# Performance work log

Hardware: AMD Instinct MI355X
Metric: run time of the kernel (lower is better)

## Reference

```python
import jax, jax.numpy as jnp
import numpy as np

N = 100000      # nodes
E = 1600000     # edges (avg degree 16)
IN = 128        # in_channels
OUT = 32        # out_channels -> hidden = 2*OUT = 64


def gcn_conv(x, src, dst, W, b):
    """PyG GCNConv: linear transform, add self loops, symmetric D^-1/2 (A+I) D^-1/2 aggregation."""
    n = x.shape[0]
    h = x @ W                                   # [N, out]
    # degree with self loops (all edge weights = 1)
    deg = jax.ops.segment_sum(jnp.ones(src.shape[0], h.dtype), dst, num_segments=n) + 1.0
    dinv = jax.lax.rsqrt(deg)                   # [N]
    norm = dinv[src] * dinv[dst]                # [E]
    agg = jax.ops.segment_sum(h[src] * norm[:, None], dst, num_segments=n)
    agg = agg + h * (dinv * dinv)[:, None]      # self-loop contribution
    return agg + b


def setup_inputs() -> dict:
    key = jax.random.key(0)
    ks = jax.random.split(key, 8)
    x = jax.random.normal(ks[0], (N, IN), jnp.float32)
    edge_index = jax.random.randint(ks[1], (2, E), 0, N, jnp.int32)
    H = 2 * OUT
    W1 = jax.random.normal(ks[2], (IN, H), jnp.float32) / jnp.sqrt(jnp.float32(IN))
    b1 = jnp.zeros((H,), jnp.float32)
    W_mu = jax.random.normal(ks[3], (H, OUT), jnp.float32) / jnp.sqrt(jnp.float32(H))
    b_mu = jnp.zeros((OUT,), jnp.float32)
    W_logstd = jax.random.normal(ks[4], (H, OUT), jnp.float32) / jnp.sqrt(jnp.float32(H))
    b_logstd = jnp.zeros((OUT,), jnp.float32)
    return {"x": x, "edge_index": edge_index, "W1": W1, "b1": b1,
            "W_mu": W_mu, "b_mu": b_mu, "W_logstd": W_logstd, "b_logstd": b_logstd}


def reference(x, edge_index, W1, b1, W_mu, b_mu, W_logstd, b_logstd):
    src, dst = edge_index[0], edge_index[1]
    h = jax.nn.relu(gcn_conv(x, src, dst, W1, b1))          # [N, 2*OUT]
    mu = gcn_conv(h, src, dst, W_mu, b_mu)                  # [N, OUT]
    logstd = gcn_conv(h, src, dst, W_logstd, b_logstd)      # [N, OUT]
    return mu, logstd
```

## Files before the change

kernel.cpp:

```cpp
#include <hip/hip_runtime.h>
#include <hip/hip_fp16.h>

#define IN_C 128
#define H 64
#define NBITS 9
#define BSZ 512
#define CHUNK 2048
#define KC 32

typedef unsigned int u32;

__device__ inline int excl_scan256(int v, int* wsum, int tid) {
    int lane = tid & 63, wid = tid >> 6;
    int s = v;
    #pragma unroll
    for (int off = 1; off < 64; off <<= 1) {
        int t = __shfl_up(s, off);
        if (lane >= off) s += t;
    }
    if (lane == 63) wsum[wid] = s;
    __syncthreads();
    if (tid == 0) {
        int c = 0;
        #pragma unroll
        for (int i = 0; i < 4; ++i) { int t = wsum[i]; wsum[i] = c; c += t; }
    }
    __syncthreads();
    return s - v + wsum[wid];
}

__device__ inline int excl_scan512(int v, int* wsum, int tid) {
    int lane = tid & 63, wid = tid >> 6;
    int s = v;
    #pragma unroll
    for (int off = 1; off < 64; off <<= 1) {
        int t = __shfl_up(s, off);
        if (lane >= off) s += t;
    }
    if (lane == 63) wsum[wid] = s;
    __syncthreads();
    if (tid == 0) {
        int c = 0;
        #pragma unroll
        for (int i = 0; i < 8; ++i) { int t = wsum[i]; wsum[i] = c; c += t; }
    }
    __syncthreads();
    return s - v + wsum[wid];
}


__global__ __launch_bounds__(256) void k_hist(const int* __restrict__ dst,
                                              int* __restrict__ bucketCnt, int E) {
    __shared__ int lh[256];
    int tid = threadIdx.x;
    lh[tid] = 0;
    __syncthreads();
    int stride = gridDim.x * 256;
    for (int i = blockIdx.x * 256 + tid; i < E; i += stride)
        atomicAdd(&lh[dst[i] >> NBITS], 1);
    __syncthreads();
    if (lh[tid]) atomicAdd(&bucketCnt[tid], lh[tid]);
}

__global__ __launch_bounds__(256) void k_bscan(const int* __restrict__ bucketCnt,
                                               int* __restrict__ bucketStart,
                                               int* __restrict__ bucketFill, int NBUK,
                                               __half* __restrict__ z0,
                                               __half* __restrict__ z1) {
    __shared__ int wsum[4];
    int tid = threadIdx.x;
    int v = (tid < NBUK) ? bucketCnt[tid] : 0;
    int ex = excl_scan256(v, wsum, tid);
    bucketStart[tid] = ex;
    if (tid == 255) bucketStart[256] = ex + v;
    bucketFill[tid] = 0;
    if (tid < H) { z0[tid] = __float2half(0.f); z1[tid] = __float2half(0.f); }
}

__global__ __launch_bounds__(256) void k_bin(const int* __restrict__ src,
                                             const int* __restrict__ dst,
                                             const int* __restrict__ bucketStart,
                                             int* __restrict__ bucketFill,
                                             u32* __restrict__ binned, int E) {
    __shared__ u32 staged[CHUNK];
    __shared__ unsigned char stagedB[CHUNK];
    __shared__ int lhist[256], lbase[256], gbase[256], lfill[256], sStart[256];
    __shared__ int wsum[4];
    int tid = threadIdx.x;
    int kbeg = blockIdx.x * CHUNK;
    int cnt = min(CHUNK, E - kbeg);
    lhist[tid] = 0; lfill[tid] = 0;
    sStart[tid] = bucketStart[tid];
    __syncthreads();
    for (int t = tid; t < cnt; t += 256)
        atomicAdd(&lhist[dst[kbeg + t] >> NBITS], 1);
    __syncthreads();
    int v = lhist[tid];
    int ex = excl_scan256(v, wsum, tid);
    lbase[tid] = ex;
    gbase[tid] = atomicAdd(&bucketFill[tid], v);
    __syncthreads();
    for (int t = tid; t < cnt; t += 256) {
        int d = dst[kbeg + t];
        int s = src[kbeg + t];
        int bk = d >> NBITS;
        int p = lbase[bk] + atomicAdd(&lfill[bk], 1);
        staged[p] = ((u32)(d & (BSZ - 1)) << 23) | (u32)s;
        stagedB[p] = (unsigned char)bk;
    }
    __syncthreads();
    for (int t = tid; t < cnt; t += 256) {
        int bk = stagedB[t];
        int gpos = sStart[bk] + gbase[bk] + (t - lbase[bk]);
        binned[gpos] = staged[t];
    }
}

__global__ __launch_bounds__(512) void k_bucket(const u32* __restrict__ binned,
                                                const int* __restrict__ bucketStart,
                                                int* __restrict__ rowptr,
                                                float* __restrict__ dinvp,
                                                int* __restrict__ colidx, int n, int E) {
    __shared__ int cnt[BSZ];
    __shared__ int loff[BSZ];
    __shared__ int wsum[8];
    int b = blockIdx.x, tid = threadIdx.x;
    int nbase = b << NBITS;
    int ebeg = bucketStart[b], eend = bucketStart[b + 1];
    cnt[tid] = 0;
    __syncthreads();
    for (int e = ebeg + tid; e < eend; e += 512)
        atomicAdd(&cnt[binned[e] >> 23], 1);
    __syncthreads();
    int c0 = cnt[tid];
    int ex = excl_scan512(c0, wsum, tid);
    loff[tid] = ex;
    int node0 = nbase + tid;
    if (node0 < n) { rowptr[node0] = ebeg + ex; dinvp[node0] = rsqrtf((float)c0 + 1.0f); }
    if (b == 0 && tid == 0) rowptr[n] = E;
    __syncthreads();
    cnt[tid] = 0;
    __syncthreads();
    for (int e = ebeg + tid; e < eend; e += 512) {
        u32 p = binned[e];
        int ln = p >> 23;
        int pos = ebeg + loff[ln] + atomicAdd(&cnt[ln], 1);
        colidx[pos] = (int)(p & 0x7FFFFF);
    }
}


__global__ __launch_bounds__(256) void k_mm1(const float* __restrict__ x,
                                             const float* __restrict__ W1,
                                             const float* __restrict__ dinv,
                                             __half* __restrict__ out, int n) {
    __shared__ float sW[KC * 64];
    __shared__ float sxT[KC * 66];
    int tid = threadIdx.x;
    int base = blockIdx.x * 64;
    const float4* W4 = (const float4*)W1;
    const float4* x4 = (const float4*)x;
    int lane = tid & 63, wave = tid >> 6;
    int c0 = (lane & 15) << 2;
    int r0 = (wave << 4) | ((lane >> 4) << 2);
    float acc[4][4] = {};

    for (int kc = 0; kc < IN_C; kc += KC) {
        __syncthreads();
        for (int t = tid; t < KC * 16; t += 256)
            ((float4*)sW)[t] = W4[(kc + (t >> 4)) * 16 + (t & 15)];
        for (int t = tid; t < 512; t += 256) {
            int node = t >> 3, kq = t & 7;
            int gn = base + node;
            float4 vv = make_float4(0.f, 0.f, 0.f, 0.f);
            if (gn < n) vv = x4[(size_t)gn * 32 + (kc >> 2) + kq];
            int kl = kq << 2;
            sxT[(kl + 0) * 66 + node] = vv.x;
            sxT[(kl + 1) * 66 + node] = vv.y;
            sxT[(kl + 2) * 66 + node] = vv.z;
            sxT[(kl + 3) * 66 + node] = vv.w;
        }
        __syncthreads();
        #pragma unroll 8
        for (int k = 0; k < KC; ++k) {
            float2 xa = *(const float2*)&sxT[k * 66 + r0];
            float2 xb = *(const float2*)&sxT[k * 66 + r0 + 2];
            float4 wv = *(const float4*)&sW[k * 64 + c0];
            acc[0][0] += xa.x * wv.x; acc[0][1] += xa.x * wv.y; acc[0][2] += xa.x * wv.z; acc[0][3] += xa.x * wv.w;
            acc[1][0] += xa.y * wv.x; acc[1][1] += xa.y * wv.y; acc[1][2] += xa.y * wv.z; acc[1][3] += xa.y * wv.w;
            acc[2][0] += xb.x * wv.x; acc[2][1] += xb.x * wv.y; acc[2][2] += xb.x * wv.z; acc[2][3] += xb.x * wv.w;
            acc[3][0] += xb.y * wv.x; acc[3][1] += xb.y * wv.y; acc[3][2] += xb.y * wv.z; acc[3][3] += xb.y * wv.w;
        }
    }
    #pragma unroll
    for (int i = 0; i < 4; ++i) {
        int node = base + r0 + i;
        if (node < n) {
            float di = dinv[node];
            union { uint2 u; __half2 h[2]; } pk;
            pk.h[0] = __floats2half2_rn(acc[i][0] * di, acc[i][1] * di);
            pk.h[1] = __floats2half2_rn(acc[i][2] * di, acc[i][3] * di);
            *(uint2*)&out[(size_t)node * 64 + c0] = pk.u;
        }
    }
}

template <bool L1, typename OutT>
__global__ __launch_bounds__(256) void k_gather(const __half* __restrict__ hs,
                                                OutT* __restrict__ out,
                                                const int* __restrict__ rowptr,
                                                const int* __restrict__ colidx,
                                                const float* __restrict__ dinv,
                                                const float* __restrict__ bias, int n) {
    int node = blockIdx.x * 4 + (threadIdx.x >> 6);
    if (node >= n) return;
    int lane = threadIdx.x & 63;
    int es = lane >> 4;
    int cc = lane & 15;
    int beg = rowptr[node];
    int end = rowptr[node + 1];
    int deg = end - beg;
    const uint2* hs4 = (const uint2*)hs;
    union U { uint2 u; __half2 h[2]; };

    int ci = (lane < deg) ? colidx[beg + lane] : n;
    U selfr; selfr.u = hs4[(size_t)node * 16 + cc];
    float a0 = 0.f, a1 = 0.f, a2 = 0.f, a3 = 0.f;

    int m = min(deg, 64);
    {
        U r[4];
        #pragma unroll
        for (int j = 0; j < 4; ++j) {
            int s = __shfl(ci, 4 * j + es);
            r[j].u = hs4[(size_t)s * 16 + cc];
        }
        #pragma unroll
        for (int j = 0; j < 4; ++j) {
            float2 f0 = __half22float2(r[j].h[0]);
            float2 f1 = __half22float2(r[j].h[1]);
            a0 += f0.x; a1 += f0.y; a2 += f1.x; a3 += f1.y;
        }
    }
    if (m > 16) {
        U r[4];
        #pragma unroll
        for (int j = 4; j < 8; ++j) {
            int s = __shfl(ci, 4 * j + es);
            r[j - 4].u = hs4[(size_t)s * 16 + cc];
        }
        #pragma unroll
        for (int j = 0; j < 4; ++j) {
            float2 f0 = __half22float2(r[j].h[0]);
            float2 f1 = __half22float2(r[j].h[1]);
            a0 += f0.x; a1 += f0.y; a2 += f1.x; a3 += f1.y;
        }
    }
    if (m > 32) {
        U r[8];
        #pragma unroll
        for (int j = 8; j < 16; ++j) {
            int s = __shfl(ci, 4 * j + es);
            r[j - 8].u = hs4[(size_t)s * 16 + cc];
        }
        #pragma unroll
        for (int j = 0; j < 8; ++j) {
            float2 f0 = __half22float2(r[j].h[0]);
            float2 f1 = __half22float2(r[j].h[1]);
            a0 += f0.x; a1 += f0.y; a2 += f1.x; a3 += f1.y;
        }
    }
    for (int e = beg + 64 + es; e < end; e += 4) {
        U r; r.u = hs4[(size_t)colidx[e] * 16 + cc];
        float2 f0 = __half22float2(r.h[0]);
        float2 f1 = __half22float2(r.h[1]);
        a0 += f0.x; a1 += f0.y; a2 += f1.x; a3 += f1.y;
    }
    a0 += __shfl_xor(a0, 16); a1 += __shfl_xor(a1, 16);
    a2 += __shfl_xor(a2, 16); a3 += __shfl_xor(a3, 16);
    a0 += __shfl_xor(a0, 32); a1 += __shfl_xor(a1, 32);
    a2 += __shfl_xor(a2, 32); a3 += __shfl_xor(a3, 32);

    if (lane < 16) {
        float2 f0 = __half22float2(selfr.h[0]);
        float2 f1 = __half22float2(selfr.h[1]);
        a0 += f0.x; a1 += f0.y; a2 += f1.x; a3 += f1.y;
        float di = dinv[node];
        float v0 = di * a0, v1 = di * a1, v2 = di * a2, v3 = di * a3;
        if (L1) {
            float4 bv = ((const float4*)bias)[cc];
            v0 = fmaxf(v0 + bv.x, 0.f) * di;
            v1 = fmaxf(v1 + bv.y, 0.f) * di;
            v2 = fmaxf(v2 + bv.z, 0.f) * di;
            v3 = fmaxf(v3 + bv.w, 0.f) * di;
        }
        if constexpr (sizeof(OutT) == 2) {
            U o;
            o.h[0] = __floats2half2_rn(v0, v1);
            o.h[1] = __floats2half2_rn(v2, v3);
            ((uint2*)out)[(size_t)node * 16 + cc] = o.u;
        } else {
            ((float4*)out)[(size_t)node * 16 + cc] = make_float4(v0, v1, v2, v3);
        }
    }
}

__global__ __launch_bounds__(256) void k_mm2(const float* __restrict__ g,
                                             const float* __restrict__ Wmu,
                                             const float* __restrict__ Wls,
                                             const float* __restrict__ bmu,
                                             const float* __restrict__ bls,
                                             float* __restrict__ out, int n) {
    __shared__ float sW[KC * 64];
    __shared__ float sgT[KC * 66];
    __shared__ float sb[64];
    int tid = threadIdx.x;
    int base = blockIdx.x * 64;
    if (tid < 64) sb[tid] = (tid < 32) ? bmu[tid] : bls[tid - 32];
    int lane = tid & 63, wave = tid >> 6;
    int c0 = (lane & 15) << 2;
    int r0 = (wave << 4) | ((lane >> 4) << 2);
    float acc[4][4] = {};

    for (int kc = 0; kc < H; kc += KC) {
        __syncthreads();
        for (int t = tid; t < KC * 16; t += 256) {
            int k = kc + (t >> 4), c = (t & 15) << 2;
            const float* srcp = (c < 32) ? (Wmu + k * 32 + c) : (Wls + k * 32 + (c - 32));
            ((float4*)sW)[t] = *(const float4*)srcp;
        }
        for (int t = tid; t < 512; t += 256) {
            int node = t >> 3, kq = t & 7;
            int gn = base + node;
            float4 vv = make_float4(0.f, 0.f, 0.f, 0.f);
            if (gn < n) vv = ((const float4*)g)[(size_t)gn * 16 + (kc >> 2) + kq];
            int kl = kq << 2;
            sgT[(kl + 0) * 66 + node] = vv.x;
            sgT[(kl + 1) * 66 + node] = vv.y;
            sgT[(kl + 2) * 66 + node] = vv.z;
            sgT[(kl + 3) * 66 + node] = vv.w;
        }
        __syncthreads();
        #pragma unroll 8
        for (int k = 0; k < KC; ++k) {
            float2 xa = *(const float2*)&sgT[k * 66 + r0];
            float2 xb = *(const float2*)&sgT[k * 66 + r0 + 2];
            float4 wv = *(const float4*)&sW[k * 64 + c0];
            acc[0][0] += xa.x * wv.x; acc[0][1] += xa.x * wv.y; acc[0][2] += xa.x * wv.z; acc[0][3] += xa.x * wv.w;
            acc[1][0] += xa.y * wv.x; acc[1][1] += xa.y * wv.y; acc[1][2] += xa.y * wv.z; acc[1][3] += xa.y * wv.w;
            acc[2][0] += xb.x * wv.x; acc[2][1] += xb.x * wv.y; acc[2][2] += xb.x * wv.z; acc[2][3] += xb.x * wv.w;
            acc[3][0] += xb.y * wv.x; acc[3][1] += xb.y * wv.y; acc[3][2] += xb.y * wv.z; acc[3][3] += xb.y * wv.w;
        }
    }
    #pragma unroll
    for (int i = 0; i < 4; ++i) {
        int node = base + r0 + i;
        if (node < n) {
            float4 o = make_float4(acc[i][0] + sb[c0], acc[i][1] + sb[c0 + 1],
                                   acc[i][2] + sb[c0 + 2], acc[i][3] + sb[c0 + 3]);
            if (c0 < 32) *(float4*)&out[(size_t)node * 32 + c0] = o;
            else *(float4*)&out[(size_t)n * 32 + (size_t)node * 32 + (c0 - 32)] = o;
        }
    }
}


extern "C" void kernel_launch(void* const* d_in, const int* in_sizes, int n_in,
                              void* d_out, int out_size, void* d_ws, size_t ws_size,
                              hipStream_t stream) {
    const float* x   = (const float*)d_in[0];
    const int*   ei  = (const int*)d_in[1];
    const float* W1  = (const float*)d_in[2];
    const float* b1  = (const float*)d_in[3];
    const float* Wmu = (const float*)d_in[4];
    const float* bmu = (const float*)d_in[5];
    const float* Wls = (const float*)d_in[6];
    const float* bls = (const float*)d_in[7];
    float* out = (float*)d_out;

    int n = in_sizes[0] / IN_C;
    int E = in_sizes[1] / 2;
    const int* src = ei;
    const int* dst = ei + E;
    int NBUK = (n + BSZ - 1) >> NBITS;

    char* p = (char*)d_ws;
    __half* Ah  = (__half*)p; p += (size_t)(n + 1) * H * sizeof(__half);
    __half* Bh  = (__half*)p; p += (size_t)(n + 1) * H * sizeof(__half);
    float* G    = (float*)p;  p += (size_t)n * H * sizeof(float);
    float* dinv = (float*)p;  p += (size_t)n * sizeof(float);
    int* rowptr = (int*)p;    p += (size_t)(n + 1) * sizeof(int);
    int* colidx = (int*)p;    p += (size_t)E * sizeof(int);
    u32* binned = (u32*)p;    p += (size_t)E * sizeof(u32);
    int* bucketCnt   = (int*)p; p += 256 * sizeof(int);
    int* bucketStart = (int*)p; p += 257 * sizeof(int);
    int* bucketFill  = (int*)p; p += 256 * sizeof(int);

    hipMemsetAsync(bucketCnt, 0, 256 * sizeof(int), stream);

    k_hist<<<256, 256, 0, stream>>>(dst, bucketCnt, E);
    k_bscan<<<1, 256, 0, stream>>>(bucketCnt, bucketStart, bucketFill, NBUK,
                                   Ah + (size_t)n * H, Bh + (size_t)n * H);
    k_bin<<<(E + CHUNK - 1) / CHUNK, 256, 0, stream>>>(src, dst, bucketStart, bucketFill, binned, E);
    k_bucket<<<NBUK, 512, 0, stream>>>(binned, bucketStart, rowptr, dinv, colidx, n, E);

    k_mm1<<<(n + 63) / 64, 256, 0, stream>>>(x, W1, dinv, Ah, n);
    k_gather<true, __half><<<(n + 3) / 4, 256, 0, stream>>>(Ah, Bh, rowptr, colidx, dinv, b1, n);
    k_gather<false, float><<<(n + 3) / 4, 256, 0, stream>>>(Bh, G, rowptr, colidx, dinv, nullptr, n);
    k_mm2<<<(n + 63) / 64, 256, 0, stream>>>(G, Wmu, Wls, bmu, bls, out, n);
}
```

Before: 282.6 us.

## Drop the histogram pass with fixed-capacity buckets and fuse binning with the first matmul

Removes the global histogram and bucket-scan kernels by giving each destination bucket a fixed capacity region (CAP slots) filled through atomic counters. Edge binning and the first x@W1 matmul now run as separate block ranges of one launch, so the matmul no longer waits for the degree computation. The source-side dinv scaling moves into the first gather as a per-edge weight. Row pointers are replaced by packed offset/degree descriptors. This cuts the launch count and serial dependencies, but costs an extra dinv gather per edge, assumes no bucket overflows CAP, and clamps the stored degree at 1023.

```diff
diff --git a/kernel.cpp b/kernel.cpp
--- a/kernel.cpp
+++ b/kernel.cpp
@@ -5,12 +5,13 @@
 #define H 64
 #define NBITS 9
 #define BSZ 512
-#define CHUNK 2048
+#define CAP 16384
+#define BINCHUNK 4096
 #define KC 32
 
 typedef unsigned int u32;
 
-__device__ inline int excl_scan256(int v, int* wsum, int tid) {
+__device__ __forceinline__ int excl_scan256(int v, int* wsum, int tid) {
     int lane = tid & 63, wid = tid >> 6;
     int s = v;
     #pragma unroll
@@ -29,7 +30,7 @@
     return s - v + wsum[wid];
 }
 
-__device__ inline int excl_scan512(int v, int* wsum, int tid) {
+__device__ __forceinline__ int excl_scan512(int v, int* wsum, int tid) {
     int lane = tid & 63, wid = tid >> 6;
     int s = v;
     #pragma unroll
@@ -48,128 +49,32 @@
     return s - v + wsum[wid];
 }
 
-
-__global__ __launch_bounds__(256) void k_hist(const int* __restrict__ dst,
-                                              int* __restrict__ bucketCnt, int E) {
-    __shared__ int lh[256];
+__global__ __launch_bounds__(256) void k_init(int* __restrict__ bucketFill,
+                                              __half* __restrict__ z0,
+                                              __half* __restrict__ z1) {
     int tid = threadIdx.x;
-    lh[tid] = 0;
-    __syncthreads();
-    int stride = gridDim.x * 256;
-    for (int i = blockIdx.x * 256 + tid; i < E; i += stride)
-        atomicAdd(&lh[dst[i] >> NBITS], 1);
-    __syncthreads();
-    if (lh[tid]) atomicAdd(&bucketCnt[tid], lh[tid]);
-}
-
-__global__ __launch_bounds__(256) void k_bscan(const int* __restrict__ bucketCnt,
-                                               int* __restrict__ bucketStart,
-                                               int* __restrict__ bucketFill, int NBUK,
-                                               __half* __restrict__ z0,
-                                               __half* __restrict__ z1) {
-    __shared__ int wsum[4];
-    int tid = threadIdx.x;
-    int v = (tid < NBUK) ? bucketCnt[tid] : 0;
-    int ex = excl_scan256(v, wsum, tid);
-    bucketStart[tid] = ex;
-    if (tid == 255) bucketStart[256] = ex + v;
     bucketFill[tid] = 0;
     if (tid < H) { z0[tid] = __float2half(0.f); z1[tid] = __float2half(0.f); }
 }
 
-__global__ __launch_bounds__(256) void k_bin(const int* __restrict__ src,
-                                             const int* __restrict__ dst,
-                                             const int* __restrict__ bucketStart,
-                                             int* __restrict__ bucketFill,
-                                             u32* __restrict__ binned, int E) {
-    __shared__ u32 staged[CHUNK];
-    __shared__ unsigned char stagedB[CHUNK];
-    __shared__ int lhist[256], lbase[256], gbase[256], lfill[256], sStart[256];
-    __shared__ int wsum[4];
-    int tid = threadIdx.x;
-    int kbeg = blockIdx.x * CHUNK;
-    int cnt = min(CHUNK, E - kbeg);
-    lhist[tid] = 0; lfill[tid] = 0;
-    sStart[tid] = bucketStart[tid];
-    __syncthreads();
-    for (int t = tid; t < cnt; t += 256)
-        atomicAdd(&lhist[dst[kbeg + t] >> NBITS], 1);
-    __syncthreads();
-    int v = lhist[tid];
-    int ex = excl_scan256(v, wsum, tid);
-    lbase[tid] = ex;
-    gbase[tid] = atomicAdd(&bucketFill[tid], v);
-    __syncthreads();
-    for (int t = tid; t < cnt; t += 256) {
-        int d = dst[kbeg + t];
-        int s = src[kbeg + t];
-        int bk = d >> NBITS;
-        int p = lbase[bk] + atomicAdd(&lfill[bk], 1);
-        staged[p] = ((u32)(d & (BSZ - 1)) << 23) | (u32)s;
-        stagedB[p] = (unsigned char)bk;
-    }
-    __syncthreads();
-    for (int t = tid; t < cnt; t += 256) {
-        int bk = stagedB[t];
-        int gpos = sStart[bk] + gbase[bk] + (t - lbase[bk]);
-        binned[gpos] = staged[t];
-    }
-}
-
-__global__ __launch_bounds__(512) void k_bucket(const u32* __restrict__ binned,
-                                                const int* __restrict__ bucketStart,
-                                                int* __restrict__ rowptr,
-                                                float* __restrict__ dinvp,
-                                                int* __restrict__ colidx, int n, int E) {
-    __shared__ int cnt[BSZ];
-    __shared__ int loff[BSZ];
-    __shared__ int wsum[8];
-    int b = blockIdx.x, tid = threadIdx.x;
-    int nbase = b << NBITS;
-    int ebeg = bucketStart[b], eend = bucketStart[b + 1];
-    cnt[tid] = 0;
-    __syncthreads();
-    for (int e = ebeg + tid; e < eend; e += 512)
-        atomicAdd(&cnt[binned[e] >> 23], 1);
-    __syncthreads();
-    int c0 = cnt[tid];
-    int ex = excl_scan512(c0, wsum, tid);
-    loff[tid] = ex;
-    int node0 = nbase + tid;
-    if (node0 < n) { rowptr[node0] = ebeg + ex; dinvp[node0] = rsqrtf((float)c0 + 1.0f); }
-    if (b == 0 && tid == 0) rowptr[n] = E;
-    __syncthreads();
-    cnt[tid] = 0;
-    __syncthreads();
-    for (int e = ebeg + tid; e < eend; e += 512) {
-        u32 p = binned[e];
-        int ln = p >> 23;
-        int pos = ebeg + loff[ln] + atomicAdd(&cnt[ln], 1);
-        colidx[pos] = (int)(p & 0x7FFFFF);
-    }
-}
-
-
-__global__ __launch_bounds__(256) void k_mm1(const float* __restrict__ x,
-                                             const float* __restrict__ W1,
-                                             const float* __restrict__ dinv,
-                                             __half* __restrict__ out, int n) {
-    __shared__ float sW[KC * 64];
-    __shared__ float sxT[KC * 66];
-    int tid = threadIdx.x;
-    int base = blockIdx.x * 64;
+__device__ __forceinline__ void mm1_tile(int tile, int t256, int n,
+                                         const float* __restrict__ x,
+                                         const float* __restrict__ W1,
+                                         __half* __restrict__ out,
+                                         float* __restrict__ sW,
+                                         float* __restrict__ sxT) {
     const float4* W4 = (const float4*)W1;
     const float4* x4 = (const float4*)x;
-    int lane = tid & 63, wave = tid >> 6;
+    int base = tile * 64;
+    int lane = t256 & 63, wave = t256 >> 6;
     int c0 = (lane & 15) << 2;
     int r0 = (wave << 4) | ((lane >> 4) << 2);
     float acc[4][4] = {};
-
     for (int kc = 0; kc < IN_C; kc += KC) {
         __syncthreads();
-        for (int t = tid; t < KC * 16; t += 256)
+        for (int t = t256; t < KC * 16; t += 256)
             ((float4*)sW)[t] = W4[(kc + (t >> 4)) * 16 + (t & 15)];
-        for (int t = tid; t < 512; t += 256) {
+        for (int t = t256; t < 512; t += 256) {
             int node = t >> 3, kq = t & 7;
             int gn = base + node;
             float4 vv = make_float4(0.f, 0.f, 0.f, 0.f);
@@ -196,19 +101,100 @@
     for (int i = 0; i < 4; ++i) {
         int node = base + r0 + i;
         if (node < n) {
-            float di = dinv[node];
             union { uint2 u; __half2 h[2]; } pk;
-            pk.h[0] = __floats2half2_rn(acc[i][0] * di, acc[i][1] * di);
-            pk.h[1] = __floats2half2_rn(acc[i][2] * di, acc[i][3] * di);
+            pk.h[0] = __floats2half2_rn(acc[i][0], acc[i][1]);
+            pk.h[1] = __floats2half2_rn(acc[i][2], acc[i][3]);
             *(uint2*)&out[(size_t)node * 64 + c0] = pk.u;
         }
+    }
+}
+
+union SMemBM {
+    struct { u32 staged[BINCHUNK]; unsigned char stagedB[BINCHUNK];
+             int lhist[256], lbase[256], gbase[256], lfill[256]; int wsum[4]; } bin;
+    struct { float sW[KC * 64]; float sxT[KC * 66]; } mm;
+};
+
+__global__ __launch_bounds__(256) void k_binmm(const int* __restrict__ src,
+                                               const int* __restrict__ dst,
+                                               int E, int n, int nbin,
+                                               int* __restrict__ bucketFill,
+                                               u32* __restrict__ binned,
+                                               const float* __restrict__ x,
+                                               const float* __restrict__ W1,
+                                               __half* __restrict__ Ah) {
+    __shared__ SMemBM sm;
+    int bid = blockIdx.x, tid = threadIdx.x;
+    if (bid < nbin) {
+        int kbeg = bid * BINCHUNK;
+        int cnt = min(BINCHUNK, E - kbeg);
+        sm.bin.lhist[tid] = 0; sm.bin.lfill[tid] = 0;
+        __syncthreads();
+        for (int t = tid; t < cnt; t += 256)
+            atomicAdd(&sm.bin.lhist[dst[kbeg + t] >> NBITS], 1);
+        __syncthreads();
+        int v = sm.bin.lhist[tid];
+        int ex = excl_scan256(v, sm.bin.wsum, tid);
+        sm.bin.lbase[tid] = ex;
+        sm.bin.gbase[tid] = v ? atomicAdd(&bucketFill[tid], v) : 0;
+        __syncthreads();
+        for (int t = tid; t < cnt; t += 256) {
+            int d = dst[kbeg + t];
+            int s = src[kbeg + t];
+            int bk = d >> NBITS;
+            int p = sm.bin.lbase[bk] + atomicAdd(&sm.bin.lfill[bk], 1);
+            sm.bin.staged[p] = ((u32)(d & (BSZ - 1)) << 23) | (u32)s;
+            sm.bin.stagedB[p] = (unsigned char)bk;
+        }
+        __syncthreads();
+        for (int t = tid; t < cnt; t += 256) {
+            int bk = sm.bin.stagedB[t];
+            binned[(size_t)bk * CAP + sm.bin.gbase[bk] + (t - sm.bin.lbase[bk])] = sm.bin.staged[t];
+        }
+    } else {
+        mm1_tile(bid - nbin, tid, n, x, W1, Ah, sm.mm.sW, sm.mm.sxT);
+    }
+}
+
+__global__ __launch_bounds__(512) void k_bucket(const u32* __restrict__ binned,
+                                                const int* __restrict__ bucketFill,
+                                                u32* __restrict__ rowdesc,
+                                                float* __restrict__ dinvp,
+                                                int* __restrict__ colidx, int n) {
+    __shared__ int cnt[BSZ];
+    __shared__ int loff[BSZ];
+    __shared__ int wsum[8];
+    int b = blockIdx.x, tid = threadIdx.x;
+    int ebeg = b * CAP;
+    int fill = bucketFill[b];
+    cnt[tid] = 0;
+    __syncthreads();
+    for (int e = tid; e < fill; e += 512)
+        atomicAdd(&cnt[binned[ebeg + e] >> 23], 1);
+    __syncthreads();
+    int c0 = cnt[tid];
+    int ex = excl_scan512(c0, wsum, tid);
+    loff[tid] = ex;
+    int node0 = (b << NBITS) + tid;
+    if (node0 < n) {
+        rowdesc[node0] = ((u32)(ebeg + ex) << 10) | (u32)min(c0, 1023);
+        dinvp[node0] = rsqrtf((float)c0 + 1.0f);
+    }
+    __syncthreads();
+    cnt[tid] = 0;
+    __syncthreads();
+    for (int e = tid; e < fill; e += 512) {
+        u32 pv = binned[ebeg + e];
+        int ln = pv >> 23;
+        int pos = ebeg + loff[ln] + atomicAdd(&cnt[ln], 1);
+        colidx[pos] = (int)(pv & 0x7FFFFF);
     }
 }
 
 template <bool L1, typename OutT>
 __global__ __launch_bounds__(256) void k_gather(const __half* __restrict__ hs,
                                                 OutT* __restrict__ out,
-                                                const int* __restrict__ rowptr,
+                                                const u32* __restrict__ rowdesc,
                                                 const int* __restrict__ colidx,
                                                 const float* __restrict__ dinv,
                                                 const float* __restrict__ bias, int n) {
@@ -217,64 +203,81 @@
     int lane = threadIdx.x & 63;
     int es = lane >> 4;
     int cc = lane & 15;
-    int beg = rowptr[node];
-    int end = rowptr[node + 1];
-    int deg = end - beg;
+    u32 rd = rowdesc[node];
+    int beg = (int)(rd >> 10);
+    int deg = (int)(rd & 1023);
+    int end = beg + deg;
     const uint2* hs4 = (const uint2*)hs;
     union U { uint2 u; __half2 h[2]; };
 
-    int ci = (lane < deg) ? colidx[beg + lane] : n;
+    int ci = n;
+    float df = 0.f;
+    if (lane < deg) {
+        ci = colidx[beg + lane];
+        if (L1) df = dinv[ci];
+    }
     U selfr; selfr.u = hs4[(size_t)node * 16 + cc];
     float a0 = 0.f, a1 = 0.f, a2 = 0.f, a3 = 0.f;
 
     int m = min(deg, 64);
     {
-        U r[4];
+        U r[4]; float d[4];
         #pragma unroll
         for (int j = 0; j < 4; ++j) {
-            int s = __shfl(ci, 4 * j + es);
+            int idx = 4 * j + es;
+            int s = __shfl(ci, idx);
+            if (L1) d[j] = __shfl(df, idx);
             r[j].u = hs4[(size_t)s * 16 + cc];
         }
         #pragma unroll
         for (int j = 0; j < 4; ++j) {
             float2 f0 = __half22float2(r[j].h[0]);
             float2 f1 = __half22float2(r[j].h[1]);
-            a0 += f0.x; a1 += f0.y; a2 += f1.x; a3 += f1.y;
+            float w = L1 ? d[j] : 1.f;
+            a0 += w * f0.x; a1 += w * f0.y; a2 += w * f1.x; a3 += w * f1.y;
         }
     }
     if (m > 16) {
-        U r[4];
+        U r[4]; float d[4];
         #pragma unroll
         for (int j = 4; j < 8; ++j) {
-            int s = __shfl(ci, 4 * j + es);
+            int idx = 4 * j + es;
+            int s = __shfl(ci, idx);
+            if (L1) d[j - 4] = __shfl(df, idx);
             r[j - 4].u = hs4[(size_t)s * 16 + cc];
         }
         #pragma unroll
         for (int j = 0; j < 4; ++j) {
             float2 f0 = __half22float2(r[j].h[0]);
             float2 f1 = __half22float2(r[j].h[1]);
-            a0 += f0.x; a1 += f0.y; a2 += f1.x; a3 += f1.y;
+            float w = L1 ? d[j] : 1.f;
+            a0 += w * f0.x; a1 += w * f0.y; a2 += w * f1.x; a3 += w * f1.y;
         }
     }
     if (m > 32) {
-        U r[8];
+        U r[8]; float d[8];
         #pragma unroll
         for (int j = 8; j < 16; ++j) {
-            int s = __shfl(ci, 4 * j + es);
+            int idx = (4 * j + es) & 63;
+            int s = __shfl(ci, idx);
+            if (L1) d[j - 8] = __shfl(df, idx);
             r[j - 8].u = hs4[(size_t)s * 16 + cc];
         }
         #pragma unroll
         for (int j = 0; j < 8; ++j) {
             float2 f0 = __half22float2(r[j].h[0]);
             float2 f1 = __half22float2(r[j].h[1]);
-            a0 += f0.x; a1 += f0.y; a2 += f1.x; a3 += f1.y;
+            float w = L1 ? d[j] : 1.f;
+            a0 += w * f0.x; a1 += w * f0.y; a2 += w * f1.x; a3 += w * f1.y;
         }
     }
     for (int e = beg + 64 + es; e < end; e += 4) {
-        U r; r.u = hs4[(size_t)colidx[e] * 16 + cc];
+        int s = colidx[e];
+        U r; r.u = hs4[(size_t)s * 16 + cc];
+        float w = L1 ? dinv[s] : 1.f;
         float2 f0 = __half22float2(r.h[0]);
         float2 f1 = __half22float2(r.h[1]);
-        a0 += f0.x; a1 += f0.y; a2 += f1.x; a3 += f1.y;
+        a0 += w * f0.x; a1 += w * f0.y; a2 += w * f1.x; a3 += w * f1.y;
     }
     a0 += __shfl_xor(a0, 16); a1 += __shfl_xor(a1, 16);
     a2 += __shfl_xor(a2, 16); a3 += __shfl_xor(a3, 16);
@@ -282,10 +285,11 @@
     a2 += __shfl_xor(a2, 32); a3 += __shfl_xor(a3, 32);
 
     if (lane < 16) {
+        float di = dinv[node];
         float2 f0 = __half22float2(selfr.h[0]);
         float2 f1 = __half22float2(selfr.h[1]);
-        a0 += f0.x; a1 += f0.y; a2 += f1.x; a3 += f1.y;
-        float di = dinv[node];
+        float ws = L1 ? di : 1.f;
+        a0 += ws * f0.x; a1 += ws * f0.y; a2 += ws * f1.x; a3 += ws * f1.y;
         float v0 = di * a0, v1 = di * a1, v2 = di * a2, v3 = di * a3;
         if (L1) {
             float4 bv = ((const float4*)bias)[cc];
@@ -380,32 +384,28 @@
 
     int n = in_sizes[0] / IN_C;
     int E = in_sizes[1] / 2;
-    const int* src = ei;
-    const int* dst = ei + E;
+    const int* srcp = ei;
+    const int* dstp = ei + E;
     int NBUK = (n + BSZ - 1) >> NBITS;
+    int nbin = (E + BINCHUNK - 1) / BINCHUNK;
+    int ntiles = (n + 63) / 64;
 
     char* p = (char*)d_ws;
     __half* Ah  = (__half*)p; p += (size_t)(n + 1) * H * sizeof(__half);
     __half* Bh  = (__half*)p; p += (size_t)(n + 1) * H * sizeof(__half);
     float* G    = (float*)p;  p += (size_t)n * H * sizeof(float);
     float* dinv = (float*)p;  p += (size_t)n * sizeof(float);
-    int* rowptr = (int*)p;    p += (size_t)(n + 1) * sizeof(int);
-    int* colidx = (int*)p;    p += (size_t)E * sizeof(int);
-    u32* binned = (u32*)p;    p += (size_t)E * sizeof(u32);
-    int* bucketCnt   = (int*)p; p += 256 * sizeof(int);
-    int* bucketStart = (int*)p; p += 257 * sizeof(int);
-    int* bucketFill  = (int*)p; p += 256 * sizeof(int);
-
-    hipMemsetAsync(bucketCnt, 0, 256 * sizeof(int), stream);
-
-    k_hist<<<256, 256, 0, stream>>>(dst, bucketCnt, E);
-    k_bscan<<<1, 256, 0, stream>>>(bucketCnt, bucketStart, bucketFill, NBUK,
-                                   Ah + (size_t)n * H, Bh + (size_t)n * H);
-    k_bin<<<(E + CHUNK - 1) / CHUNK, 256, 0, stream>>>(src, dst, bucketStart, bucketFill, binned, E);
-    k_bucket<<<NBUK, 512, 0, stream>>>(binned, bucketStart, rowptr, dinv, colidx, n, E);
-
-    k_mm1<<<(n + 63) / 64, 256, 0, stream>>>(x, W1, dinv, Ah, n);
-    k_gather<true, __half><<<(n + 3) / 4, 256, 0, stream>>>(Ah, Bh, rowptr, colidx, dinv, b1, n);
-    k_gather<false, float><<<(n + 3) / 4, 256, 0, stream>>>(Bh, G, rowptr, colidx, dinv, nullptr, n);
+    u32* rowdesc = (u32*)p;   p += (size_t)n * sizeof(u32);
+    int* colidx = (int*)p;    p += (size_t)NBUK * CAP * sizeof(int);
+    u32* binned = (u32*)p;    p += (size_t)NBUK * CAP * sizeof(u32);
+    int* bucketFill = (int*)p; p += 256 * sizeof(int);
+
+    k_init<<<1, 256, 0, stream>>>(bucketFill, Ah + (size_t)n * H, Bh + (size_t)n * H);
+    k_binmm<<<nbin + ntiles, 256, 0, stream>>>(srcp, dstp, E, n, nbin,
+                                               bucketFill, binned, x, W1, Ah);
+    k_bucket<<<NBUK, 512, 0, stream>>>(binned, bucketFill, rowdesc, dinv, colidx, n);
+
+    k_gather<true, __half><<<(n + 3) / 4, 256, 0, stream>>>(Ah, Bh, rowdesc, colidx, dinv, b1, n);
+    k_gather<false, float><<<(n + 3) / 4, 256, 0, stream>>>(Bh, G, rowdesc, colidx, dinv, nullptr, n);
     k_mm2<<<(n + 63) / 64, 256, 0, stream>>>(G, Wmu, Wls, bmu, bls, out, n);
 }
```

Measured after the change: 256.1 us. 9.4% less time.
